# Kernel tuning notes

Hardware: AMD Instinct MI355X
Metric: run time of the kernel (lower is better)

The kernel has to match this reference:

```python
import jax, jax.numpy as jnp
import numpy as np

C = 16; HP = 16; WP = 16; D = 32; KITER = 4; P = 8; N = P * P; B = 16; HID = 64


def conv2d(x, w, b):
    # x: (B, Cin, H, W), w: (Cout, Cin, kh, kw), 'same' padding for 3x3
    y = jax.lax.conv_general_dilated(x, w, (1, 1), [(1, 1), (1, 1)],
                                     dimension_numbers=('NCHW', 'OIHW', 'NCHW'))
    return y + b[None, :, None, None]


def setup_inputs() -> dict:
    key = jax.random.key(0)
    ks = jax.random.split(key, 20)
    n = lambda k, shape, s=0.1: jax.random.normal(k, shape, jnp.float32) * s
    # 4-neighbor directed grid edges over P x P nodes
    edges = []
    for p in range(P):
        for q in range(P):
            i = p * P + q
            for dp, dq in ((0, 1), (1, 0), (0, -1), (-1, 0)):
                pp, qq = p + dp, q + dq
                if 0 <= pp < P and 0 <= qq < P:
                    edges.append((i, pp * P + qq))
    edge_index = jnp.asarray(np.asarray(edges, np.int32))  # (E, 2) with (i=dst, j=src)
    return {
        'seed': n(ks[0], (B, C, P * HP, P * WP), 1.0),
        'edge_index': edge_index,
        'wq': n(ks[1], (C, D)), 'bq': jnp.zeros((D,), jnp.float32),
        'wk': n(ks[2], (C, D)), 'bk': jnp.zeros((D,), jnp.float32),
        'wm': n(ks[3], (C, C, 3, 3)), 'bm': jnp.zeros((C,), jnp.float32),
        'a_w1': n(ks[4], (2 * D, HID)), 'a_b1': jnp.zeros((HID,), jnp.float32),
        'a_w2': n(ks[5], (HID, HID)), 'a_b2': jnp.zeros((HID,), jnp.float32),
        'a_wo': n(ks[6], (HID, 1)), 'a_bo': jnp.zeros((1,), jnp.float32),
        'g_w': n(ks[7], (C, 1, 3, 3)), 'g_b': jnp.zeros((C,), jnp.float32),
        'gru_wg': n(ks[8], (2 * C, 2 * C, 3, 3)), 'gru_bg': jnp.zeros((2 * C,), jnp.float32),
        'gru_wc': n(ks[9], (C, 2 * C, 3, 3)), 'gru_bc': jnp.zeros((C,), jnp.float32),
    }


def reference(seed, edge_index, wq, bq, wk, bk, wm, bm,
              a_w1, a_b1, a_w2, a_b2, a_wo, a_bo,
              g_w, g_b, gru_wg, gru_bg, gru_wc, gru_bc):
    Bb, Cc, PH, PW = seed.shape
    Pp = PH // HP
    Nn = Pp * Pp
    # patchify: (B,C,PH,PW) -> (B,N,C,H,W), node order is row-major (p,q)
    X = seed.reshape(Bb, Cc, Pp, HP, Pp, WP).transpose(0, 2, 4, 1, 3, 5).reshape(Bb, Nn, Cc, HP, WP)
    ei = edge_index[:, 0]  # dst node i
    ej = edge_index[:, 1]  # src node j
    # GateConv on a spatially-constant map e: conv(e*ones) = e * conv(ones) (+bias).
    ones_map = jnp.ones((1, 1, HP, WP), seed.dtype)
    T = jax.lax.conv_general_dilated(ones_map, g_w, (1, 1), [(1, 1), (1, 1)],
                                     dimension_numbers=('NCHW', 'OIHW', 'NCHW'))  # (1,C,H,W)
    for _ in range(KITER):
        xm = X.mean((-2, -1))  # (B,N,C); mean commutes with the 1x1 convs f_Q/f_K
        q_vec = xm @ wq + bq   # (B,N,d)
        k_vec = xm @ wk + bk
        M = conv2d(X.reshape(Bb * Nn, Cc, HP, WP), wm, bm).reshape(Bb, Nn, Cc, HP, WP)
        # per-edge attention scores via ConcatMLP
        h0 = jnp.concatenate([q_vec[:, ei], k_vec[:, ej]], axis=-1)  # (B,E,2d)
        h1 = jax.nn.relu(h0 @ a_w1 + a_b1)
        h2 = jax.nn.relu(h1 @ a_w2 + a_b2)
        e = (h2 @ a_wo + a_bo)[..., 0]  # (B,E)
        # gate map and gated messages
        G = jax.nn.sigmoid(e[:, :, None, None, None] * T[None] + g_b[None, None, :, None, None])  # (B,E,C,H,W)
        msg = G * M[:, ej]  # gather src patches, gate
        agg = jax.ops.segment_sum(jnp.moveaxis(msg, 1, 0), ei, num_segments=Nn)  # (N,B,C,H,W)
        M_agg = jnp.moveaxis(agg, 0, 1).reshape(Bb * Nn, Cc, HP, WP)
        # ConvGRU cell update
        h = X.reshape(Bb * Nn, Cc, HP, WP)
        zr = jax.nn.sigmoid(conv2d(jnp.concatenate([M_agg, h], axis=1), gru_wg, gru_bg))
        z, r = zr[:, :Cc], zr[:, Cc:]
        cand = jnp.tanh(conv2d(jnp.concatenate([M_agg, r * h], axis=1), gru_wc, gru_bc))
        X = ((1.0 - z) * h + z * cand).reshape(Bb, Nn, Cc, HP, WP)
    # unpatchify
    out = X.reshape(Bb, Pp, Pp, Cc, HP, WP).transpose(0, 3, 1, 4, 2, 5).reshape(Bb, Cc, PH, PW)
    return out
```

## Files before the change

kernel.cpp:

```cpp
#include <hip/hip_runtime.h>
#include <hip/hip_bf16.h>

#define Bt 16
#define Ct 16
#define Nt 64
#define KITERt 4

#define WF_TOTAL 25681
#define SWZ_TOTAL 16384
#define SETUP_IDX (WF_TOTAL + 4096 + Nt + SWZ_TOTAL)
#define SAH_STRIDE 40

typedef __attribute__((ext_vector_type(8))) short bf16x8;
typedef __attribute__((ext_vector_type(4))) short s16x4;
typedef __attribute__((ext_vector_type(4))) float f32x4;

__device__ inline short f2bs(float f) {
    __hip_bfloat16 h = __float2bfloat16(f);
    short s; __builtin_memcpy(&s, &h, 2); return s;
}
__device__ inline float bs2f(short s) {
    __hip_bfloat16 h; __builtin_memcpy(&h, &s, 2);
    return __bfloat162float(h);
}
__device__ inline float loadf(const void* p, int i, int isf32) {
    return isf32 ? ((const float*)p)[i]
                 : __bfloat162float(((const __hip_bfloat16*)p)[i]);
}
__device__ inline float sigm(float x) {
    return __builtin_amdgcn_rcpf(1.f + __expf(-x));
}
__device__ inline float tanh_fast(float x) {
    float e = __expf(2.f * x);
    return 1.f - 2.f * __builtin_amdgcn_rcpf(e + 1.f);
}

__global__ __launch_bounds__(256) void setup_kernel(
    const void* __restrict__ seed,
    const void* __restrict__ wq, const void* __restrict__ bq,
    const void* __restrict__ wk, const void* __restrict__ bk,
    const void* __restrict__ wm, const void* __restrict__ bm,
    const void* __restrict__ w1, const void* __restrict__ b1,
    const void* __restrict__ w2, const void* __restrict__ b2,
    const void* __restrict__ wo, const void* __restrict__ bo,
    const void* __restrict__ gw, const void* __restrict__ gb,
    const void* __restrict__ wg, const void* __restrict__ bg,
    const void* __restrict__ wc, const void* __restrict__ bc,
    const int* __restrict__ edge, int E,
    float* __restrict__ Wf, float* __restrict__ Tswz,
    int* __restrict__ counts, int* __restrict__ nbrs,
    __hip_bfloat16* __restrict__ swz,
    short* __restrict__ Xb, float* __restrict__ qv0, float* __restrict__ kv0,
    int* __restrict__ flag)
{
    __shared__ float sred[4];
    __shared__ int sflag;
    __shared__ float xred[64];
    __shared__ int snb[256];
    int bn = blockIdx.x, t = threadIdx.x;
    int lane = t & 63, wv = t >> 6;

    {
        float v = fabsf(__bfloat162float(((const __hip_bfloat16*)seed)[t]));
        if (!(v <= 1e30f)) v = 1e30f;
#pragma unroll
        for (int off = 1; off < 64; off <<= 1) v = fmaxf(v, __shfl_xor(v, off, 64));
        if (lane == 0) sred[wv] = v;
        __syncthreads();
        if (t == 0) {
            float m = fmaxf(fmaxf(sred[0], sred[1]), fmaxf(sred[2], sred[3]));
            sflag = (m > 1e10f) ? 1 : 0;
            if (bn == 0) *flag = sflag;
        }
        __syncthreads();
    }
    int isf32 = sflag;

    if (bn == 0) {
        snb[t] = 0;
        __syncthreads();
        for (int e = t; e < E; e += 256) {
            int ei = edge[2 * e], ej = edge[2 * e + 1];
            int d = ej - ei;
            int slot = (d == 1) ? 0 : (d == 8) ? 1 : (d == -1) ? 2 : 3;
            snb[ei * 4 + slot] = ej + 1;
        }
        __syncthreads();
        if (t < 64) {
            int dcount = 0;
            int outv[4] = {0, 0, 0, 0};
#pragma unroll
            for (int s = 0; s < 4; ++s) {
                int v = snb[t * 4 + s];
                if (v) outv[dcount++] = v - 1;
            }
            counts[t] = dcount;
#pragma unroll
            for (int s = 0; s < 4; ++s) nbrs[t * 4 + s] = outv[s];
        }
    }

    int idx = bn * 256 + t;
    if (idx < WF_TOTAL) {
        int i = idx;
        const void* base;
        if (i < 512) base = wq;
        else if ((i -= 512) < 32) base = bq;
        else if ((i -= 32) < 512) base = wk;
        else if ((i -= 512) < 32) base = bk;
        else if ((i -= 32) < 2304) base = wm;
        else if ((i -= 2304) < 16) base = bm;
        else if ((i -= 16) < 4096) base = w1;
        else if ((i -= 4096) < 64) base = b1;
        else if ((i -= 64) < 4096) base = w2;
        else if ((i -= 4096) < 64) base = b2;
        else if ((i -= 64) < 64) base = wo;
        else if ((i -= 64) < 1) base = bo;
        else if ((i -= 1) < 16) base = gb;
        else if ((i -= 16) < 9216) base = wg;
        else if ((i -= 9216) < 32) base = bg;
        else if ((i -= 32) < 4608) base = wc;
        else { i -= 4608; base = bc; }
        Wf[idx] = loadf(base, i, isf32);
    } else if (idx < WF_TOTAL + 4096) {
        int j = idx - WF_TOTAL;
        int tt = j >> 4, rr = j & 15;
        int wv2 = tt >> 6, ln = tt & 63, qd = ln >> 4, nn = ln & 15;
        int mt = rr >> 2, r2 = rr & 3;
        int pix = (wv2 * 4 + mt) * 16 + qd * 4 + r2;
        int y = pix >> 4, x = pix & 15;
        float s = 0.f;
        for (int ky = 0; ky < 3; ++ky)
            for (int kx = 0; kx < 3; ++kx) {
                int yy = y + ky - 1, xx = x + kx - 1;
                if (yy >= 0 && yy < 16 && xx >= 0 && xx < 16)
                    s += loadf(gw, nn * 9 + ky * 3 + kx, isf32);
            }
        Tswz[j] = s;
    } else if (idx >= WF_TOTAL + 4096 + Nt && idx < SETUP_IDX) {
        int j = idx - (WF_TOTAL + 4096 + Nt);
        float val;
        if (j < 9216) {
            int sn = j >> 9, rem = j & 511;
            int ln = rem >> 3, jj = rem & 7;
            int s = sn >> 1, nt = sn & 1;
            int ci = (ln >> 4) * 8 + jj;
            int co = nt * 16 + (ln & 15);
            val = loadf(wg, co * 288 + ci * 9 + s, isf32);
        } else if (j < 9216 + 4608) {
            int j1 = j - 9216;
            int s = j1 >> 9, rem = j1 & 511;
            int ln = rem >> 3, jj = rem & 7;
            int ci = (ln >> 4) * 8 + jj;
            int co = ln & 15;
            val = loadf(wc, co * 288 + ci * 9 + s, isf32);
        } else {
            int j2 = j - 13824;
            int sp = j2 >> 9, rem = j2 & 511;
            int ln = rem >> 3, jj = rem & 7;
            int k = (ln >> 4) * 8 + jj;
            int s = sp * 2 + (k >> 4);
            int ci = k & 15;
            int co = ln & 15;
            val = (s <= 8) ? loadf(wm, co * 144 + ci * 9 + s, isf32) : 0.f;
        }
        swz[j] = __float2bfloat16(val);
    }

    {
        int b = bn >> 6, n = bn & 63;
        int pq = n >> 3, qq = n & 7;
        int y = t >> 4, x = t & 15;
        float v[16];
#pragma unroll
        for (int c = 0; c < 16; ++c)
            v[c] = loadf(seed, ((b * 16 + c) * 128 + pq * 16 + y) * 128 + qq * 16 + x, isf32);
        bf16x8 o0, o1;
#pragma unroll
        for (int c = 0; c < 8; ++c) { o0[c] = f2bs(v[c]); o1[c] = f2bs(v[8 + c]); }
        short* xo = Xb + bn * 4096;
        *(bf16x8*)(xo + t * 16) = o0;
        *(bf16x8*)(xo + t * 16 + 8) = o1;
#pragma unroll
        for (int c = 0; c < 16; ++c) {
            float s = v[c];
#pragma unroll
            for (int off = 1; off < 64; off <<= 1) s += __shfl_xor(s, off, 64);
            if (lane == c) xred[wv * 16 + c] = s;
        }
        __syncthreads();
        if (t < 64) {
            int d = t & 31;
            float a = (t < 32) ? loadf(bq, d, isf32) : loadf(bk, d, isf32);
#pragma unroll
            for (int c = 0; c < 16; ++c) {
                float xm = (xred[c] + xred[16 + c] + xred[32 + c] + xred[48 + c]) * (1.f / 256.f);
                a += xm * ((t < 32) ? loadf(wq, c * 32 + d, isf32)
                                    : loadf(wk, c * 32 + d, isf32));
            }
            if (t < 32) qv0[bn * 32 + d] = a; else kv0[bn * 32 + d] = a;
        }
    }
}

__global__ __launch_bounds__(256) void iter_kernel(
    const short* __restrict__ Xin, short* __restrict__ Xout,
    const float* __restrict__ qin, const float* __restrict__ kin,
    float* __restrict__ qout, float* __restrict__ kout,
    const float* __restrict__ Tswz,
    const short* __restrict__ WmS,
    const short* __restrict__ WgS,
    const short* __restrict__ WcS,
    const float* __restrict__ Wf,
    const int* __restrict__ counts, const int* __restrict__ nbrs,
    const int* __restrict__ flagp, void* __restrict__ out, int last)
{
    __shared__ __align__(16) short sAH[324 * SAH_STRIDE];
    __shared__ float evs[4];
    __shared__ float xred[64];
    int bn = blockIdx.x, b = bn >> 6, i = bn & 63;
    int t = threadIdx.x, lane = t & 63, wv = t >> 6;
    int quad = lane >> 4, n16 = lane & 15;

    int4 nb4 = *(const int4*)(nbrs + i * 4);
    int deg = counts[i];
    int ejl[4] = {nb4.x, nb4.y, nb4.z, nb4.w};
    bf16x8 nbA0, nbA1, nbB0, nbB1;
    if (deg > 0) {
        const short* mp = Xin + (b * 64 + ejl[0]) * 4096 + t * 16;
        nbA0 = *(const bf16x8*)(mp);
        nbA1 = *(const bf16x8*)(mp + 8);
    }

    float T_lane[16];
#pragma unroll
    for (int r = 0; r < 16; ++r) T_lane[r] = Tswz[t * 16 + r];
    float gb_l = Wf[11793 + n16];
    float bm_l = Wf[3392 + n16];

    const short* xown = Xin + bn * 4096;

    for (int p = t; p < 324; p += 256) {
        int yy = p / 18 - 1, xx = p % 18 - 1;
        short* row = sAH + p * SAH_STRIDE;
        if ((unsigned)yy < 16u && (unsigned)xx < 16u) {
            const short* src = xown + (yy * 16 + xx) * 16;
            *(bf16x8*)(row + 16) = *(const bf16x8*)(src);
            *(bf16x8*)(row + 24) = *(const bf16x8*)(src + 8);
        } else {
            bf16x8 z = {0, 0, 0, 0, 0, 0, 0, 0};
            *(bf16x8*)(row) = z;      *(bf16x8*)(row + 8) = z;
            *(bf16x8*)(row + 16) = z; *(bf16x8*)(row + 24) = z;
        }
    }

    if (wv < deg) {
        int ej = ejl[wv];
        float h0 = (lane < 32) ? qin[bn * 32 + lane]
                               : kin[(b * 64 + ej) * 32 + (lane - 32)];
        const float* W1 = Wf + 3408;
        const float* W2 = Wf + 7568;
        float p0 = 0.f, p1 = 0.f, p2 = 0.f, p3 = 0.f;
#pragma unroll
        for (int j = 0; j < 64; j += 4) {
            p0 += __shfl(h0, j + 0, 64) * W1[(j + 0) * 64 + lane];
            p1 += __shfl(h0, j + 1, 64) * W1[(j + 1) * 64 + lane];
            p2 += __shfl(h0, j + 2, 64) * W1[(j + 2) * 64 + lane];
            p3 += __shfl(h0, j + 3, 64) * W1[(j + 3) * 64 + lane];
        }
        float a1 = fmaxf(Wf[7504 + lane] + ((p0 + p1) + (p2 + p3)), 0.f);
        p0 = p1 = p2 = p3 = 0.f;
#pragma unroll
        for (int j = 0; j < 64; j += 4) {
            p0 += __shfl(a1, j + 0, 64) * W2[(j + 0) * 64 + lane];
            p1 += __shfl(a1, j + 1, 64) * W2[(j + 1) * 64 + lane];
            p2 += __shfl(a1, j + 2, 64) * W2[(j + 2) * 64 + lane];
            p3 += __shfl(a1, j + 3, 64) * W2[(j + 3) * 64 + lane];
        }
        float a2 = fmaxf(Wf[11664 + lane] + ((p0 + p1) + (p2 + p3)), 0.f);
        float pe = a2 * Wf[11728 + lane];
#pragma unroll
        for (int off = 32; off; off >>= 1) pe += __shfl_down(pe, off, 64);
        if (lane == 0) evs[wv] = pe + Wf[11792];
    }
    __syncthreads();

    f32x4 magg[4];
#pragma unroll
    for (int mt = 0; mt < 4; ++mt) magg[mt] = (f32x4){0.f, 0.f, 0.f, 0.f};
    int pp = ((t >> 4) + 1) * 18 + (t & 15) + 1;
    for (int ii = 0; ii < deg; ++ii) {
        *(bf16x8*)(sAH + pp * SAH_STRIDE) = nbA0;
        *(bf16x8*)(sAH + pp * SAH_STRIDE + 8) = nbA1;
        if (ii + 1 < deg) {
            const short* mp = Xin + (b * 64 + ejl[ii + 1]) * 4096 + t * 16;
            nbB0 = *(const bf16x8*)(mp);
            nbB1 = *(const bf16x8*)(mp + 8);
        }
        __syncthreads();
        float evv = evs[ii];
        f32x4 acc[4];
#pragma unroll
        for (int mt = 0; mt < 4; ++mt) acc[mt] = (f32x4){bm_l, bm_l, bm_l, bm_l};
#pragma unroll
        for (int sp = 0; sp < 5; ++sp) {
            bf16x8 Bf = *(const bf16x8*)(WmS + sp * 512 + lane * 8);
            int s2 = sp * 2 + (quad >> 1);
            if (s2 > 8) s2 = 8;
            int ky = s2 / 3, kx = s2 - (s2 / 3) * 3;
            int cib = (quad & 1) * 8;
#pragma unroll
            for (int mt = 0; mt < 4; ++mt) {
                int pc = (wv * 4 + mt + ky) * 18 + n16 + kx;
                bf16x8 A = *(const bf16x8*)(sAH + pc * SAH_STRIDE + cib);
                acc[mt] = __builtin_amdgcn_mfma_f32_16x16x32_bf16(A, Bf, acc[mt], 0, 0, 0);
            }
        }
#pragma unroll
        for (int mt = 0; mt < 4; ++mt)
#pragma unroll
            for (int r = 0; r < 4; ++r)
                magg[mt][r] += sigm(evv * T_lane[mt * 4 + r] + gb_l) * acc[mt][r];
        nbA0 = nbB0; nbA1 = nbB1;
        __syncthreads();
    }
#pragma unroll
    for (int mt = 0; mt < 4; ++mt)
#pragma unroll
        for (int r = 0; r < 4; ++r) {
            int p = (wv * 4 + mt + 1) * 18 + quad * 4 + r + 1;
            sAH[p * SAH_STRIDE + n16] = f2bs(magg[mt][r]);
        }
    __syncthreads();

    float bz = Wf[21025 + n16], br = Wf[21025 + 16 + n16];
    f32x4 accZ[4], accR[4];
#pragma unroll
    for (int mt = 0; mt < 4; ++mt) {
        accZ[mt] = (f32x4){bz, bz, bz, bz};
        accR[mt] = (f32x4){br, br, br, br};
    }
#pragma unroll
    for (int s = 0; s < 9; ++s) {
        int ky = s / 3, kx = s - (s / 3) * 3;
        bf16x8 B0 = *(const bf16x8*)(WgS + (s * 2 + 0) * 512 + lane * 8);
        bf16x8 B1 = *(const bf16x8*)(WgS + (s * 2 + 1) * 512 + lane * 8);
#pragma unroll
        for (int mt = 0; mt < 4; ++mt) {
            int pc = (wv * 4 + mt + ky) * 18 + n16 + kx;
            bf16x8 A = *(const bf16x8*)(sAH + pc * SAH_STRIDE + quad * 8);
            accZ[mt] = __builtin_amdgcn_mfma_f32_16x16x32_bf16(A, B0, accZ[mt], 0, 0, 0);
            accR[mt] = __builtin_amdgcn_mfma_f32_16x16x32_bf16(A, B1, accR[mt], 0, 0, 0);
        }
    }
    float zf[16], hf[16], rh[16];
#pragma unroll
    for (int mt = 0; mt < 4; ++mt)
#pragma unroll
        for (int r = 0; r < 4; ++r) {
            int k = mt * 4 + r;
            int ps = (wv * 4 + mt + 1) * 18 + quad * 4 + r + 1;
            hf[k] = bs2f(sAH[ps * SAH_STRIDE + 16 + n16]);
            zf[k] = sigm(accZ[mt][r]);
            rh[k] = sigm(accR[mt][r]) * hf[k];
        }
    __syncthreads();
#pragma unroll
    for (int mt = 0; mt < 4; ++mt)
#pragma unroll
        for (int r = 0; r < 4; ++r) {
            int ps = (wv * 4 + mt + 1) * 18 + quad * 4 + r + 1;
            sAH[ps * SAH_STRIDE + 16 + n16] = f2bs(rh[mt * 4 + r]);
        }
    __syncthreads();

    float bcl = Wf[25665 + n16];
    f32x4 accC[4];
#pragma unroll
    for (int mt = 0; mt < 4; ++mt) accC[mt] = (f32x4){bcl, bcl, bcl, bcl};
#pragma unroll
    for (int s = 0; s < 9; ++s) {
        int ky = s / 3, kx = s - (s / 3) * 3;
        bf16x8 Bc = *(const bf16x8*)(WcS + s * 512 + lane * 8);
#pragma unroll
        for (int mt = 0; mt < 4; ++mt) {
            int pc = (wv * 4 + mt + ky) * 18 + n16 + kx;
            bf16x8 A = *(const bf16x8*)(sAH + pc * SAH_STRIDE + quad * 8);
            accC[mt] = __builtin_amdgcn_mfma_f32_16x16x32_bf16(A, Bc, accC[mt], 0, 0, 0);
        }
    }
    float nxv[16];
#pragma unroll
    for (int mt = 0; mt < 4; ++mt)
#pragma unroll
        for (int r = 0; r < 4; ++r) {
            int k = mt * 4 + r;
            nxv[k] = (1.f - zf[k]) * hf[k] + zf[k] * tanh_fast(accC[mt][r]);
        }

    if (!last) {
        short* xo = Xout + bn * 4096;
        float ssum = 0.f;
#pragma unroll
        for (int mt = 0; mt < 4; ++mt)
#pragma unroll
            for (int r = 0; r < 4; ++r) {
                int k = mt * 4 + r;
                ssum += nxv[k];
                int pix = (wv * 4 + mt) * 16 + quad * 4 + r;
                xo[pix * 16 + n16] = f2bs(nxv[k]);
            }
        ssum += __shfl_xor(ssum, 16, 64);
        ssum += __shfl_xor(ssum, 32, 64);
        if (lane < 16) xred[wv * 16 + lane] = ssum;
        __syncthreads();
        if (t < 64) {
            int d = t & 31;
            const float* W = (t < 32) ? Wf : Wf + 544;
            float a = (t < 32) ? Wf[512 + d] : Wf[1056 + d];
#pragma unroll
            for (int c = 0; c < 16; ++c) {
                float xc = (xred[c] + xred[16 + c] + xred[32 + c] + xred[48 + c]) * (1.f / 256.f);
                a += xc * W[c * 32 + d];
            }
            if (t < 32) qout[bn * 32 + d] = a; else kout[bn * 32 + d] = a;
        }
    } else {
        int isf32 = *flagp;
        int pq = i >> 3, qq = i & 7;
#pragma unroll
        for (int mt = 0; mt < 4; ++mt) {
            long base = ((long)(b * 16 + n16) * 128 + pq * 16 + wv * 4 + mt) * 128
                        + qq * 16 + quad * 4;
            if (isf32) {
                f32x4 v = {nxv[mt * 4], nxv[mt * 4 + 1], nxv[mt * 4 + 2], nxv[mt * 4 + 3]};
                *(f32x4*)((float*)out + base) = v;
            } else {
                s16x4 v = {f2bs(nxv[mt * 4]), f2bs(nxv[mt * 4 + 1]),
                           f2bs(nxv[mt * 4 + 2]), f2bs(nxv[mt * 4 + 3])};
                *(s16x4*)((short*)out + base) = v;
            }
        }
    }
}

extern "C" void kernel_launch(void* const* d_in, const int* in_sizes, int n_in,
                              void* d_out, int out_size, void* d_ws, size_t ws_size,
                              hipStream_t stream)
{
    const void* seed = d_in[0];
    const int* edge = (const int*)d_in[1];
    int E = in_sizes[1] / 2;

    float* ws = (float*)d_ws;
    short* Xb0 = (short*)ws;
    short* Xb1 = (short*)(ws + 2097152);
    float* qv0 = ws + 4194304;
    float* kv0 = qv0 + 32768;
    float* qv1 = kv0 + 32768;
    float* kv1 = qv1 + 32768;
    float* Tswz = kv1 + 32768;
    float* Wf = Tswz + 4096;
    int* nbrs = (int*)(ws + 4355168);
    int* counts = nbrs + 256;
    int* flag = counts + 64;
    __hip_bfloat16* swz = (__hip_bfloat16*)(ws + 4355600);

    const short* WgS = (const short*)swz;
    const short* WcS = (const short*)(swz + 9216);
    const short* WmS = (const short*)(swz + 13824);

    setup_kernel<<<Bt * Nt, 256, 0, stream>>>(
        seed,
        d_in[2], d_in[3], d_in[4], d_in[5], d_in[6], d_in[7], d_in[8], d_in[9],
        d_in[10], d_in[11], d_in[12], d_in[13], d_in[14], d_in[15], d_in[16],
        d_in[17], d_in[18], d_in[19],
        edge, E, Wf, Tswz, counts, nbrs, swz, Xb0, qv0, kv0, flag);

    short* Xs[2] = {Xb0, Xb1};
    float* qs[2] = {qv0, qv1};
    float* ks[2] = {kv0, kv1};
    for (int it = 0; it < KITERt; ++it) {
        int in = it & 1, on = in ^ 1;
        int last = (it == KITERt - 1);
        iter_kernel<<<Bt * Nt, 256, 0, stream>>>(
            Xs[in], Xs[on], qs[in], ks[in], qs[on], ks[on],
            Tswz, WmS, WgS, WcS, Wf, counts, nbrs, flag, d_out, last);
    }
}
```

Baseline: 230.2 us.

## Compute message conv once per node instead of per incoming edge

Before, each block recomputed the 3x3 message convolution on every neighbor patch it gathered, up to four convs per node per iteration. Now each node's message map M is computed once, in the setup kernel for the first iteration and at the end of the previous iteration otherwise, and stored to global memory in fp32. The aggregation then becomes a per-pixel gated sum over the precomputed neighbor M tiles. This cuts MFMA work and barriers in the aggregation loop, at the cost of extra fp32 global traffic (reading up to four 16 KB neighbor tiles and writing one per block) and a larger workspace.

Result: slower. 453.9 us (+97.2%).

```diff
diff --git a/kernel.cpp b/kernel.cpp
--- a/kernel.cpp
+++ b/kernel.cpp
@@ -47,18 +47,21 @@
     const void* __restrict__ wg, const void* __restrict__ bg,
     const void* __restrict__ wc, const void* __restrict__ bc,
     const int* __restrict__ edge, int E,
-    float* __restrict__ Wf, float* __restrict__ Tswz,
+    float* __restrict__ Wf, float* __restrict__ Tpix,
     int* __restrict__ counts, int* __restrict__ nbrs,
     __hip_bfloat16* __restrict__ swz,
     short* __restrict__ Xb, float* __restrict__ qv0, float* __restrict__ kv0,
+    float* __restrict__ M0,
     int* __restrict__ flag)
 {
     __shared__ float sred[4];
     __shared__ int sflag;
     __shared__ float xred[64];
     __shared__ int snb[256];
+    __shared__ __align__(16) short sM[324 * SAH_STRIDE];
     int bn = blockIdx.x, t = threadIdx.x;
     int lane = t & 63, wv = t >> 6;
+    int quad = lane >> 4, n16 = lane & 15;
 
     {
         float v = fabsf(__bfloat162float(((const __hip_bfloat16*)seed)[t]));
@@ -124,19 +127,16 @@
         Wf[idx] = loadf(base, i, isf32);
     } else if (idx < WF_TOTAL + 4096) {
         int j = idx - WF_TOTAL;
-        int tt = j >> 4, rr = j & 15;
-        int wv2 = tt >> 6, ln = tt & 63, qd = ln >> 4, nn = ln & 15;
-        int mt = rr >> 2, r2 = rr & 3;
-        int pix = (wv2 * 4 + mt) * 16 + qd * 4 + r2;
+        int pix = j >> 4, ch = j & 15;
         int y = pix >> 4, x = pix & 15;
         float s = 0.f;
         for (int ky = 0; ky < 3; ++ky)
             for (int kx = 0; kx < 3; ++kx) {
                 int yy = y + ky - 1, xx = x + kx - 1;
                 if (yy >= 0 && yy < 16 && xx >= 0 && xx < 16)
-                    s += loadf(gw, nn * 9 + ky * 3 + kx, isf32);
-            }
-        Tswz[j] = s;
+                    s += loadf(gw, ch * 9 + ky * 3 + kx, isf32);
+            }
+        Tpix[j] = s;
     } else if (idx >= WF_TOTAL + 4096 + Nt && idx < SETUP_IDX) {
         int j = idx - (WF_TOTAL + 4096 + Nt);
         float val;
@@ -181,6 +181,19 @@
         short* xo = Xb + bn * 4096;
         *(bf16x8*)(xo + t * 16) = o0;
         *(bf16x8*)(xo + t * 16 + 8) = o1;
+
+        for (int p = t; p < 324; p += 256) {
+            int yy = p / 18 - 1, xx = p % 18 - 1;
+            if (!((unsigned)yy < 16u && (unsigned)xx < 16u)) {
+                bf16x8 z = {0, 0, 0, 0, 0, 0, 0, 0};
+                *(bf16x8*)(sM + p * SAH_STRIDE) = z;
+                *(bf16x8*)(sM + p * SAH_STRIDE + 8) = z;
+            }
+        }
+        int pp = ((t >> 4) + 1) * 18 + (t & 15) + 1;
+        *(bf16x8*)(sM + pp * SAH_STRIDE) = o0;
+        *(bf16x8*)(sM + pp * SAH_STRIDE + 8) = o1;
+
 #pragma unroll
         for (int c = 0; c < 16; ++c) {
             float s = v[c];
@@ -200,14 +213,49 @@
             }
             if (t < 32) qv0[bn * 32 + d] = a; else kv0[bn * 32 + d] = a;
         }
+
+        float bm_l = loadf(bm, n16, isf32);
+        f32x4 accM[4];
+#pragma unroll
+        for (int mt = 0; mt < 4; ++mt) accM[mt] = (f32x4){bm_l, bm_l, bm_l, bm_l};
+#pragma unroll
+        for (int sp = 0; sp < 5; ++sp) {
+            int s2 = sp * 2 + (quad >> 1);
+            int valid = (s2 <= 8);
+            int s2c = valid ? s2 : 8;
+            int ky = s2c / 3, kx = s2c - ky * 3;
+            bf16x8 Bf;
+#pragma unroll
+            for (int j = 0; j < 8; ++j) {
+                short bv = 0;
+                if (valid) bv = f2bs(loadf(wm, n16 * 144 + ((quad & 1) * 8 + j) * 9 + s2, isf32));
+                Bf[j] = bv;
+            }
+            int cib = (quad & 1) * 8;
+#pragma unroll
+            for (int mt = 0; mt < 4; ++mt) {
+                int pc = (wv * 4 + mt + ky) * 18 + n16 + kx;
+                bf16x8 A = *(const bf16x8*)(sM + pc * SAH_STRIDE + cib);
+                accM[mt] = __builtin_amdgcn_mfma_f32_16x16x32_bf16(A, Bf, accM[mt], 0, 0, 0);
+            }
+        }
+        float* mo = M0 + bn * 4096;
+#pragma unroll
+        for (int mt = 0; mt < 4; ++mt)
+#pragma unroll
+            for (int r = 0; r < 4; ++r) {
+                int pix = (wv * 4 + mt) * 16 + quad * 4 + r;
+                mo[pix * 16 + n16] = accM[mt][r];
+            }
     }
 }
 
 __global__ __launch_bounds__(256) void iter_kernel(
     const short* __restrict__ Xin, short* __restrict__ Xout,
+    const float* __restrict__ Min, float* __restrict__ Mout,
     const float* __restrict__ qin, const float* __restrict__ kin,
     float* __restrict__ qout, float* __restrict__ kout,
-    const float* __restrict__ Tswz,
+    const float* __restrict__ Tpix,
     const short* __restrict__ WmS,
     const short* __restrict__ WgS,
     const short* __restrict__ WcS,
@@ -221,21 +269,28 @@
     int bn = blockIdx.x, b = bn >> 6, i = bn & 63;
     int t = threadIdx.x, lane = t & 63, wv = t >> 6;
     int quad = lane >> 4, n16 = lane & 15;
+    int pp = ((t >> 4) + 1) * 18 + (t & 15) + 1;
 
     int4 nb4 = *(const int4*)(nbrs + i * 4);
     int deg = counts[i];
     int ejl[4] = {nb4.x, nb4.y, nb4.z, nb4.w};
-    bf16x8 nbA0, nbA1, nbB0, nbB1;
-    if (deg > 0) {
-        const short* mp = Xin + (b * 64 + ejl[0]) * 4096 + t * 16;
-        nbA0 = *(const bf16x8*)(mp);
-        nbA1 = *(const bf16x8*)(mp + 8);
-    }
-
-    float T_lane[16];
-#pragma unroll
-    for (int r = 0; r < 16; ++r) T_lane[r] = Tswz[t * 16 + r];
-    float gb_l = Wf[11793 + n16];
+    f32x4 nm[4][4];
+#pragma unroll
+    for (int ii = 0; ii < 4; ++ii)
+        if (ii < deg) {
+            const float* mp = Min + (b * 64 + ejl[ii]) * 4096 + t * 16;
+            nm[ii][0] = *(const f32x4*)(mp);
+            nm[ii][1] = *(const f32x4*)(mp + 4);
+            nm[ii][2] = *(const f32x4*)(mp + 8);
+            nm[ii][3] = *(const f32x4*)(mp + 12);
+        }
+
+    float Tp[16], gbv[16];
+#pragma unroll
+    for (int c = 0; c < 16; ++c) {
+        Tp[c] = Tpix[t * 16 + c];
+        gbv[c] = Wf[11793 + c];
+    }
     float bm_l = Wf[3392 + n16];
 
     const short* xown = Xin + bn * 4096;
@@ -285,52 +340,24 @@
     }
     __syncthreads();
 
-    f32x4 magg[4];
-#pragma unroll
-    for (int mt = 0; mt < 4; ++mt) magg[mt] = (f32x4){0.f, 0.f, 0.f, 0.f};
-    int pp = ((t >> 4) + 1) * 18 + (t & 15) + 1;
-    for (int ii = 0; ii < deg; ++ii) {
-        *(bf16x8*)(sAH + pp * SAH_STRIDE) = nbA0;
-        *(bf16x8*)(sAH + pp * SAH_STRIDE + 8) = nbA1;
-        if (ii + 1 < deg) {
-            const short* mp = Xin + (b * 64 + ejl[ii + 1]) * 4096 + t * 16;
-            nbB0 = *(const bf16x8*)(mp);
-            nbB1 = *(const bf16x8*)(mp + 8);
-        }
-        __syncthreads();
-        float evv = evs[ii];
-        f32x4 acc[4];
-#pragma unroll
-        for (int mt = 0; mt < 4; ++mt) acc[mt] = (f32x4){bm_l, bm_l, bm_l, bm_l};
-#pragma unroll
-        for (int sp = 0; sp < 5; ++sp) {
-            bf16x8 Bf = *(const bf16x8*)(WmS + sp * 512 + lane * 8);
-            int s2 = sp * 2 + (quad >> 1);
-            if (s2 > 8) s2 = 8;
-            int ky = s2 / 3, kx = s2 - (s2 / 3) * 3;
-            int cib = (quad & 1) * 8;
-#pragma unroll
-            for (int mt = 0; mt < 4; ++mt) {
-                int pc = (wv * 4 + mt + ky) * 18 + n16 + kx;
-                bf16x8 A = *(const bf16x8*)(sAH + pc * SAH_STRIDE + cib);
-                acc[mt] = __builtin_amdgcn_mfma_f32_16x16x32_bf16(A, Bf, acc[mt], 0, 0, 0);
-            }
-        }
-#pragma unroll
-        for (int mt = 0; mt < 4; ++mt)
-#pragma unroll
-            for (int r = 0; r < 4; ++r)
-                magg[mt][r] += sigm(evv * T_lane[mt * 4 + r] + gb_l) * acc[mt][r];
-        nbA0 = nbB0; nbA1 = nbB1;
-        __syncthreads();
-    }
-#pragma unroll
-    for (int mt = 0; mt < 4; ++mt)
-#pragma unroll
-        for (int r = 0; r < 4; ++r) {
-            int p = (wv * 4 + mt + 1) * 18 + quad * 4 + r + 1;
-            sAH[p * SAH_STRIDE + n16] = f2bs(magg[mt][r]);
-        }
+    float magg[16];
+#pragma unroll
+    for (int c = 0; c < 16; ++c) magg[c] = 0.f;
+#pragma unroll
+    for (int ii = 0; ii < 4; ++ii)
+        if (ii < deg) {
+            float evv = evs[ii];
+#pragma unroll
+            for (int c = 0; c < 16; ++c)
+                magg[c] += sigm(evv * Tp[c] + gbv[c]) * nm[ii][c >> 2][c & 3];
+        }
+    {
+        bf16x8 mg0, mg1;
+#pragma unroll
+        for (int c = 0; c < 8; ++c) { mg0[c] = f2bs(magg[c]); mg1[c] = f2bs(magg[c + 8]); }
+        *(bf16x8*)(sAH + pp * SAH_STRIDE) = mg0;
+        *(bf16x8*)(sAH + pp * SAH_STRIDE + 8) = mg1;
+    }
     __syncthreads();
 
     float bz = Wf[21025 + n16], br = Wf[21025 + 16 + n16];
@@ -398,34 +425,7 @@
             nxv[k] = (1.f - zf[k]) * hf[k] + zf[k] * tanh_fast(accC[mt][r]);
         }
 
-    if (!last) {
-        short* xo = Xout + bn * 4096;
-        float ssum = 0.f;
-#pragma unroll
-        for (int mt = 0; mt < 4; ++mt)
-#pragma unroll
-            for (int r = 0; r < 4; ++r) {
-                int k = mt * 4 + r;
-                ssum += nxv[k];
-                int pix = (wv * 4 + mt) * 16 + quad * 4 + r;
-                xo[pix * 16 + n16] = f2bs(nxv[k]);
-            }
-        ssum += __shfl_xor(ssum, 16, 64);
-        ssum += __shfl_xor(ssum, 32, 64);
-        if (lane < 16) xred[wv * 16 + lane] = ssum;
-        __syncthreads();
-        if (t < 64) {
-            int d = t & 31;
-            const float* W = (t < 32) ? Wf : Wf + 544;
-            float a = (t < 32) ? Wf[512 + d] : Wf[1056 + d];
-#pragma unroll
-            for (int c = 0; c < 16; ++c) {
-                float xc = (xred[c] + xred[16 + c] + xred[32 + c] + xred[48 + c]) * (1.f / 256.f);
-                a += xc * W[c * 32 + d];
-            }
-            if (t < 32) qout[bn * 32 + d] = a; else kout[bn * 32 + d] = a;
-        }
-    } else {
+    if (last) {
         int isf32 = *flagp;
         int pq = i >> 3, qq = i & 7;
 #pragma unroll
@@ -441,6 +441,69 @@
                 *(s16x4*)((short*)out + base) = v;
             }
         }
+        return;
+    }
+
+    __syncthreads();
+
+    float ssum = 0.f;
+#pragma unroll
+    for (int mt = 0; mt < 4; ++mt)
+#pragma unroll
+        for (int r = 0; r < 4; ++r) {
+            int k = mt * 4 + r;
+            ssum += nxv[k];
+            int p = (wv * 4 + mt + 1) * 18 + quad * 4 + r + 1;
+            sAH[p * SAH_STRIDE + n16] = f2bs(nxv[k]);
+        }
+    ssum += __shfl_xor(ssum, 16, 64);
+    ssum += __shfl_xor(ssum, 32, 64);
+    if (lane < 16) xred[wv * 16 + lane] = ssum;
+    __syncthreads();
+
+    f32x4 accM[4];
+#pragma unroll
+    for (int mt = 0; mt < 4; ++mt) accM[mt] = (f32x4){bm_l, bm_l, bm_l, bm_l};
+#pragma unroll
+    for (int sp = 0; sp < 5; ++sp) {
+        bf16x8 Bf = *(const bf16x8*)(WmS + sp * 512 + lane * 8);
+        int s2 = sp * 2 + (quad >> 1);
+        if (s2 > 8) s2 = 8;
+        int ky = s2 / 3, kx = s2 - (s2 / 3) * 3;
+        int cib = (quad & 1) * 8;
+#pragma unroll
+        for (int mt = 0; mt < 4; ++mt) {
+            int pc = (wv * 4 + mt + ky) * 18 + n16 + kx;
+            bf16x8 A = *(const bf16x8*)(sAH + pc * SAH_STRIDE + cib);
+            accM[mt] = __builtin_amdgcn_mfma_f32_16x16x32_bf16(A, Bf, accM[mt], 0, 0, 0);
+        }
+    }
+    {
+        float* mo = Mout + bn * 4096;
+#pragma unroll
+        for (int mt = 0; mt < 4; ++mt)
+#pragma unroll
+            for (int r = 0; r < 4; ++r) {
+                int pix = (wv * 4 + mt) * 16 + quad * 4 + r;
+                mo[pix * 16 + n16] = accM[mt][r];
+            }
+    }
+    {
+        const short* row = sAH + pp * SAH_STRIDE;
+        short* xo = Xout + bn * 4096 + t * 16;
+        *(bf16x8*)(xo) = *(const bf16x8*)(row);
+        *(bf16x8*)(xo + 8) = *(const bf16x8*)(row + 8);
+    }
+    if (t < 64) {
+        int d = t & 31;
+        const float* W = (t < 32) ? Wf : Wf + 544;
+        float a = (t < 32) ? Wf[512 + d] : Wf[1056 + d];
+#pragma unroll
+        for (int c = 0; c < 16; ++c) {
+            float xc = (xred[c] + xred[16 + c] + xred[32 + c] + xred[48 + c]) * (1.f / 256.f);
+            a += xc * W[c * 32 + d];
+        }
+        if (t < 32) qout[bn * 32 + d] = a; else kout[bn * 32 + d] = a;
     }
 }
 
@@ -459,12 +522,14 @@
     float* kv0 = qv0 + 32768;
     float* qv1 = kv0 + 32768;
     float* kv1 = qv1 + 32768;
-    float* Tswz = kv1 + 32768;
-    float* Wf = Tswz + 4096;
+    float* Tpix = kv1 + 32768;
+    float* Wf = Tpix + 4096;
     int* nbrs = (int*)(ws + 4355168);
     int* counts = nbrs + 256;
     int* flag = counts + 64;
     __hip_bfloat16* swz = (__hip_bfloat16*)(ws + 4355600);
+    float* Mb0 = ws + 4363792;
+    float* Mb1 = ws + 8558096;
 
     const short* WgS = (const short*)swz;
     const short* WcS = (const short*)(swz + 9216);
@@ -475,16 +540,17 @@
         d_in[2], d_in[3], d_in[4], d_in[5], d_in[6], d_in[7], d_in[8], d_in[9],
         d_in[10], d_in[11], d_in[12], d_in[13], d_in[14], d_in[15], d_in[16],
         d_in[17], d_in[18], d_in[19],
-        edge, E, Wf, Tswz, counts, nbrs, swz, Xb0, qv0, kv0, flag);
+        edge, E, Wf, Tpix, counts, nbrs, swz, Xb0, qv0, kv0, Mb0, flag);
 
     short* Xs[2] = {Xb0, Xb1};
+    float* Ms[2] = {Mb0, Mb1};
     float* qs[2] = {qv0, qv1};
     float* ks[2] = {kv0, kv1};
     for (int it = 0; it < KITERt; ++it) {
         int in = it & 1, on = in ^ 1;
         int last = (it == KITERt - 1);
         iter_kernel<<<Bt * Nt, 256, 0, stream>>>(
-            Xs[in], Xs[on], qs[in], ks[in], qs[on], ks[on],
-            Tswz, WmS, WgS, WcS, Wf, counts, nbrs, flag, d_out, last);
-    }
-}
+            Xs[in], Xs[on], Ms[in], Ms[on], qs[in], ks[in], qs[on], ks[on],
+            Tpix, WmS, WgS, WcS, Wf, counts, nbrs, flag, d_out, last);
+    }
+}
```
